# Kernel tuning notes

Measured on AMD Instinct MI355X. Metric: run time of the kernel, lower is better.

## Reference

```python
import jax, jax.numpy as jnp
import numpy as np

N, E, B = 20000, 60000, 512
F_IN, ED, H, C = 7, 3, 4, 256
HC = H * C  # 1024
D_MODEL = 1024
EPS_BN = 1e-5


def setup_inputs() -> dict:
    key = jax.random.key(0)
    ks = jax.random.split(key, 24)
    s = 0.05
    inp = {
        'x': jax.random.normal(ks[0], (N, F_IN), jnp.float32),
        'edge_index': jax.random.randint(ks[1], (2, E), 0, N, jnp.int32),
        'edge_attr': jax.random.normal(ks[2], (E, ED), jnp.float32),
        'batch': jnp.sort(jax.random.randint(ks[3], (N,), 0, B, jnp.int32)),
        'w0': jax.random.normal(ks[4], (F_IN, HC), jnp.float32) * s,
        'w_rest': jax.random.normal(ks[5], (3, HC, HC), jnp.float32) * s,
        'w_edge': jax.random.normal(ks[6], (4, ED, HC), jnp.float32) * s,
        'att_src': jax.random.normal(ks[7], (4, H, C), jnp.float32) * s,
        'att_dst': jax.random.normal(ks[8], (4, H, C), jnp.float32) * s,
        'att_edge': jax.random.normal(ks[9], (4, H, C), jnp.float32) * s,
        'bias012': jax.random.normal(ks[10], (3, HC), jnp.float32) * s,
        'bias3': jax.random.normal(ks[11], (C,), jnp.float32) * s,
        'bn_gamma': jnp.ones((3, HC), jnp.float32),
        'bn_beta': jnp.zeros((3, HC), jnp.float32),
        'bn_mean': jnp.zeros((3, HC), jnp.float32),
        'bn_var': jnp.ones((3, HC), jnp.float32),
        'gate_w': jax.random.normal(ks[12], (C, 1), jnp.float32) * s,
        'gate_b': jnp.zeros((1,), jnp.float32),
        'proj_w': jax.random.normal(ks[13], (C, D_MODEL), jnp.float32) * s,
        'proj_b': jnp.zeros((D_MODEL,), jnp.float32),
    }
    return inp


def _gat_layer(x, ei, ea, W, We, a_s, a_d, a_e, bias, concat):
    # PyG GATConv with edge_dim, add_self_loops=True (fill_value='mean'), eval mode (no dropout)
    n = x.shape[0]
    sl = jnp.arange(n, dtype=ei.dtype)
    ea_mean = ea.mean(axis=0)
    ei = jnp.concatenate([ei, jnp.stack([sl, sl])], axis=1)            # [2, E+N]
    ea = jnp.concatenate([ea, jnp.broadcast_to(ea_mean, (n, ea.shape[1]))], axis=0)
    h = (x @ W).reshape(n, H, C)                                       # [N,H,C]
    alpha_src = jnp.einsum('nhc,hc->nh', h, a_s)
    alpha_dst = jnp.einsum('nhc,hc->nh', h, a_d)
    eh = (ea @ We).reshape(-1, H, C)
    alpha_e = jnp.einsum('ehc,hc->eh', eh, a_e)
    src, dst = ei[0], ei[1]
    alpha = jax.nn.leaky_relu(alpha_src[src] + alpha_dst[dst] + alpha_e, 0.2)  # [E+N,H]
    amax = jax.ops.segment_max(alpha, dst, num_segments=n)
    alpha = jnp.exp(alpha - amax[dst])
    denom = jax.ops.segment_sum(alpha, dst, num_segments=n)
    alpha = alpha / (denom[dst] + 1e-16)
    msg = h[src] * alpha[:, :, None]                                   # [E+N,H,C]
    out = jax.ops.segment_sum(msg, dst, num_segments=n)                # [N,H,C]
    out = out.reshape(n, H * C) if concat else out.mean(axis=1)
    return out + bias


def reference(x, edge_index, edge_attr, batch, w0, w_rest, w_edge, att_src, att_dst,
              att_edge, bias012, bias3, bn_gamma, bn_beta, bn_mean, bn_var,
              gate_w, gate_b, proj_w, proj_b):
    h = x
    for i in range(4):
        W = w0 if i == 0 else w_rest[i - 1]
        concat = i < 3
        b = bias012[i] if concat else bias3
        h = _gat_layer(h, edge_index, edge_attr, W, w_edge[i],
                       att_src[i], att_dst[i], att_edge[i], b, concat)
        if i < 3:
            # BatchNorm1d in eval mode, then ReLU (dropout is identity in eval)
            h = (h - bn_mean[i]) * (bn_gamma[i] / jnp.sqrt(bn_var[i] + EPS_BN)) + bn_beta[i]
            h = jax.nn.relu(h)
    # AttentionalAggregation: segment softmax over gate scores, weighted sum per graph
    gate = h @ gate_w + gate_b                                         # [N,1]
    gmax = jax.ops.segment_max(gate, batch, num_segments=B)
    g = jnp.exp(gate - gmax[batch])
    gsum = jax.ops.segment_sum(g, batch, num_segments=B)
    w = g / (gsum[batch] + 1e-16)
    graph = jax.ops.segment_sum(w * h, batch, num_segments=B)          # [B,256]
    return graph @ proj_w + proj_b                                     # [B,1024]
```

## Files before the change

kernel.cpp:

```cpp
#include <hip/hip_runtime.h>
#include <math.h>

#define NN 20000
#define NP 20480
#define EE 60000
#define BB 512
#define HC 1024
#define HH 4
#define CC 256

typedef _Float16 f16;
typedef f16 half8 __attribute__((ext_vector_type(8)));
typedef f16 f16x4 __attribute__((ext_vector_type(4)));
typedef float floatx4 __attribute__((ext_vector_type(4)));
typedef float floatx16 __attribute__((ext_vector_type(16)));

__device__ __forceinline__ size_t af_off(int n, int c) {
    int mblk = n >> 7, rr = n & 127;
    int iter = c >> 5, kc = c & 31;
    int kh = kc >> 4, kg = (kc >> 3) & 1, e = kc & 7;
    return ((((size_t)(mblk * 32 + iter) * 2 + kh) * 4 + (rr >> 5)) * 64 +
            (kg * 32 + (rr & 31))) * 8 + e;
}

__global__ void ea_sum_kernel(const float* __restrict__ ea, float* sums, int E_) {
    float s0 = 0.f, s1 = 0.f, s2 = 0.f;
    for (int e = blockIdx.x * 256 + threadIdx.x; e < E_; e += gridDim.x * 256) {
        s0 += ea[e * 3 + 0];
        s1 += ea[e * 3 + 1];
        s2 += ea[e * 3 + 2];
    }
    for (int o = 32; o; o >>= 1) {
        s0 += __shfl_down(s0, o);
        s1 += __shfl_down(s1, o);
        s2 += __shfl_down(s2, o);
    }
    if ((threadIdx.x & 63) == 0) {
        atomicAdd(&sums[0], s0);
        atomicAdd(&sums[1], s1);
        atomicAdd(&sums[2], s2);
    }
}

__global__ void hist_kernel(const int* __restrict__ ei, int* counts, int E_) {
    int e = blockIdx.x * 256 + threadIdx.x;
    if (e < E_) atomicAdd(&counts[ei[E_ + e]], 1);
}

__global__ void scan1_kernel(const int* __restrict__ counts, int* __restrict__ partial,
                             int* __restrict__ psums, int n) {
    __shared__ int sdata[256];
    int t = threadIdx.x;
    int i = blockIdx.x * 256 + t;
    int v = (i < n) ? counts[i] : 0;
    sdata[t] = v;
    __syncthreads();
#pragma unroll
    for (int off = 1; off < 256; off <<= 1) {
        int tmp = (t >= off) ? sdata[t - off] : 0;
        __syncthreads();
        sdata[t] += tmp;
        __syncthreads();
    }
    if (i < n) partial[i] = sdata[t];
    if (t == 255) psums[blockIdx.x] = sdata[255];
}

__global__ void scan2_kernel(int* __restrict__ psums, int nb) {
    __shared__ int sdata[128];
    int t = threadIdx.x;
    sdata[t] = (t < nb) ? psums[t] : 0;
    __syncthreads();
#pragma unroll
    for (int off = 1; off < 128; off <<= 1) {
        int tmp = (t >= off) ? sdata[t - off] : 0;
        __syncthreads();
        sdata[t] += tmp;
        __syncthreads();
    }
    if (t < nb) psums[t] = (t == 0) ? 0 : sdata[t - 1];
}

__global__ void scan3_kernel(const int* __restrict__ partial, const int* __restrict__ psums,
                             int* __restrict__ indptr, int n) {
    int i = blockIdx.x * 256 + threadIdx.x;
    if (i == 0) indptr[0] = 0;
    if (i < n) indptr[i + 1] = partial[i] + psums[blockIdx.x];
}

__global__ void scatter_kernel(const int* __restrict__ ei, const int* __restrict__ indptr,
                               int* fill, int* sorted, int* sdst, int E_) {
    int e = blockIdx.x * 256 + threadIdx.x;
    if (e >= E_) return;
    int d = ei[E_ + e];
    int pos = indptr[d] + atomicAdd(&fill[d], 1);
    sorted[pos] = e;
    sdst[pos] = d;
}

__global__ void bptr_kernel(const int* __restrict__ batch, int* bptr, int n, int nb) {
    int i = blockIdx.x * 256 + threadIdx.x;
    if (i >= n) return;
    int b = batch[i];
    if (i == 0) {
        for (int bb = 0; bb <= b; bb++) bptr[bb] = 0;
    } else {
        int pb = batch[i - 1];
        if (pb != b) {
            for (int bb = pb + 1; bb <= b; bb++) bptr[bb] = i;
        }
    }
    if (i == n - 1) {
        for (int bb = b + 1; bb <= nb; bb++) bptr[bb] = n;
    }
}

__global__ void wconv_kernel(const float* __restrict__ w_rest, f16* __restrict__ wt) {
    __shared__ float tile[64][65];
    int l = blockIdx.z;
    int bx = blockIdx.x * 64;
    int by = blockIdx.y * 64;
    int t = threadIdx.x;
    int tr = t >> 6, tc = t & 63;
#pragma unroll
    for (int i = 0; i < 16; i++) {
        int r = by + i * 4 + tr;
        tile[i * 4 + tr][tc] = w_rest[(size_t)l * 1048576 + (size_t)r * 1024 + bx + tc];
    }
    __syncthreads();
#pragma unroll
    for (int i = 0; i < 16; i++) {
        int n = bx + i * 4 + tr;
        wt[(size_t)l * 1048576 + (size_t)n * 1024 + by + tc] = (f16)tile[tc][i * 4 + tr];
    }
}

__global__ void bfrs_kernel(const f16* __restrict__ wt, f16* __restrict__ Bf) {
    int iter = blockIdx.x, nblk = blockIdx.y, l = blockIdx.z;
    const f16* wl = wt + (size_t)l * 1048576;
    f16* bl = Bf + (size_t)l * 1048576;
    int t = threadIdx.x;
    for (int c = t; c < 512; c += 256) {
        int kh = c >> 8, rem = c & 255, cg = rem >> 6, lane = rem & 63;
        int n = nblk * 128 + cg * 32 + (lane & 31);
        int k = iter * 32 + (kh * 2 + (lane >> 5)) * 8;
        half8 v = *(const half8*)&wl[(size_t)n * 1024 + k];
        *(half8*)&bl[(size_t)(nblk * 32 + iter) * 4096 + c * 8] = v;
    }
}

__global__ void mmat_all_kernel(const float* __restrict__ w_edge,
                                const float* __restrict__ att_edge,
                                const float* __restrict__ ea_sums, float* Mmat,
                                float* ae_self, float invE) {
    __shared__ float red[256];
    __shared__ float Ms[12];
    int l = blockIdx.x;
    int t = threadIdx.x;
    for (int dh = 0; dh < 12; dh++) {
        int d = dh >> 2, hh = dh & 3;
        float v = w_edge[l * 3072 + d * HC + hh * CC + t] * att_edge[l * HC + hh * CC + t];
        red[t] = v;
        __syncthreads();
        for (int o = 128; o; o >>= 1) {
            if (t < o) red[t] += red[t + o];
            __syncthreads();
        }
        if (t == 0) {
            Ms[dh] = red[0];
            Mmat[l * 12 + dh] = red[0];
        }
        __syncthreads();
    }
    if (t < 4) {
        float v = 0.f;
        for (int d = 0; d < 3; d++) v += ea_sums[d] * invE * Ms[d * 4 + t];
        ae_self[l * 4 + t] = v;
    }
}

__global__ void pack_kernel(const int* __restrict__ ei, const int* __restrict__ sorted,
                            const float* __restrict__ ea, const float* __restrict__ Mmat,
                            int* __restrict__ ssrc, float* __restrict__ aeh_pk) {
    int idx = blockIdx.x * 256 + threadIdx.x;
    if (idx >= EE) return;
    int eid = sorted[idx];
    ssrc[idx] = ei[eid];
    float a0 = ea[eid * 3 + 0], a1 = ea[eid * 3 + 1], a2 = ea[eid * 3 + 2];
#pragma unroll
    for (int l = 0; l < 4; l++) {
#pragma unroll
        for (int h = 0; h < 4; h++) {
            aeh_pk[(size_t)idx * 16 + l * 4 + h] =
                a0 * Mmat[l * 12 + h] + a1 * Mmat[l * 12 + 4 + h] + a2 * Mmat[l * 12 + 8 + h];
        }
    }
}

__global__ void edgep_kernel(const int* __restrict__ ssrc, const int* __restrict__ sdst,
                             const float* __restrict__ aeh_pk, const float* __restrict__ asrc,
                             const float* __restrict__ adst, float* __restrict__ pe,
                             int layer) {
    int i = blockIdx.x * 256 + threadIdx.x;
    if (i >= EE) return;
    int src = ssrc[i];
    int dst = sdst[i];
    float4 a = *(const float4*)&asrc[(size_t)src * 4];
    float4 d = *(const float4*)&adst[(size_t)dst * 4];
    float4 m = *(const float4*)&aeh_pk[(size_t)i * 16 + layer * 4];
    float r[4] = {a.x + d.x + m.x, a.y + d.y + m.y, a.z + d.z + m.z, a.w + d.w + m.w};
    float4 o;
#pragma unroll
    for (int k = 0; k < 4; k++) {
        float v = (r[k] > 0.f) ? r[k] : 0.2f * r[k];
        (&o.x)[k] = __expf(v);
    }
    *(float4*)&pe[(size_t)i * 4] = o;
}

__global__ void bnss_kernel(const float* __restrict__ bias012, const float* __restrict__ bn_g,
                            const float* __restrict__ bn_b, const float* __restrict__ bn_m,
                            const float* __restrict__ bn_v, float2* __restrict__ bnss) {
    int i = blockIdx.x * 256 + threadIdx.x;
    if (i >= 3 * HC) return;
    float s = bn_g[i] * rsqrtf(bn_v[i] + 1e-5f);
    float2 o;
    o.x = s;
    o.y = (bias012[i] - bn_m[i]) * s + bn_b[i];
    bnss[i] = o;
}

__global__ void wvec_kernel(const float* __restrict__ w_rest, const float* __restrict__ att_src,
                            const float* __restrict__ att_dst, float* __restrict__ wsv,
                            float* __restrict__ wdv) {
    int l = blockIdx.y;
    int k = blockIdx.x;
    int t = threadIdx.x;
    int hp = t >> 6, lane = t & 63;
    int col = hp * 256 + lane * 4;
    const float* wrow = w_rest + (size_t)l * 1048576 + (size_t)k * 1024;
    float4 w4 = *(const float4*)&wrow[col];
    float4 a4 = *(const float4*)&att_src[(l + 1) * HC + col];
    float4 d4 = *(const float4*)&att_dst[(l + 1) * HC + col];
    float sp = w4.x * a4.x + w4.y * a4.y + w4.z * a4.z + w4.w * a4.w;
    float dp = w4.x * d4.x + w4.y * d4.y + w4.z * d4.z + w4.w * d4.w;
    for (int m = 1; m < 64; m <<= 1) {
        sp += __shfl_xor(sp, m);
        dp += __shfl_xor(dp, m);
    }
    if (lane == 0) {
        wsv[((size_t)l * 1024 + k) * 4 + hp] = sp;
        wdv[((size_t)l * 1024 + k) * 4 + hp] = dp;
    }
}

__global__ void w0vec_kernel(const float* __restrict__ w0, const float* __restrict__ att_src,
                             const float* __restrict__ att_dst, float* __restrict__ w0s,
                             float* __restrict__ w0d) {
    int f = blockIdx.x;
    int t = threadIdx.x;
    int hp = t >> 6, lane = t & 63;
    int col = hp * 256 + lane * 4;
    float4 w4 = *(const float4*)&w0[f * HC + col];
    float4 a4 = *(const float4*)&att_src[col];
    float4 d4 = *(const float4*)&att_dst[col];
    float sp = w4.x * a4.x + w4.y * a4.y + w4.z * a4.z + w4.w * a4.w;
    float dp = w4.x * d4.x + w4.y * d4.y + w4.z * d4.z + w4.w * d4.w;
    for (int m = 1; m < 64; m <<= 1) {
        sp += __shfl_xor(sp, m);
        dp += __shfl_xor(dp, m);
    }
    if (lane == 0) {
        w0s[f * 4 + hp] = sp;
        w0d[f * 4 + hp] = dp;
    }
}

__global__ void alpha0_kernel(const float* __restrict__ x, const float* __restrict__ w0s,
                              const float* __restrict__ w0d, float* __restrict__ asrc,
                              float* __restrict__ adst) {
    int n = blockIdx.x * 256 + threadIdx.x;
    if (n >= NN) return;
    float xr[7];
#pragma unroll
    for (int f = 0; f < 7; f++) xr[f] = x[n * 7 + f];
#pragma unroll
    for (int hp = 0; hp < 4; hp++) {
        float s = 0.f, d = 0.f;
#pragma unroll
        for (int f = 0; f < 7; f++) {
            s += xr[f] * w0s[f * 4 + hp];
            d += xr[f] * w0d[f * 4 + hp];
        }
        asrc[n * 4 + hp] = s;
        adst[n * 4 + hp] = d;
    }
}

__global__ void agg0x_kernel(const float* __restrict__ x, const float* __restrict__ asrc,
                             const float* __restrict__ adst, const float* __restrict__ ae_self,
                             const int* __restrict__ ssrc, const float* __restrict__ pe,
                             const int* __restrict__ indptr, float* __restrict__ xagg) {
    int n = blockIdx.x * 256 + threadIdx.x;
    if (n >= NN) return;
    float4 as4 = *(const float4*)&asrc[(size_t)n * 4];
    float4 ad4 = *(const float4*)&adst[(size_t)n * 4];
    float adl[4] = {ad4.x, ad4.y, ad4.z, ad4.w};
    float asl[4] = {as4.x, as4.y, as4.z, as4.w};
    float xr[7];
#pragma unroll
    for (int f = 0; f < 7; f++) xr[f] = x[n * 7 + f];
    float denom[4];
    float xa[4][7];
#pragma unroll
    for (int h = 0; h < 4; h++) {
        float r = asl[h] + adl[h] + ae_self[h];
        r = (r > 0.f) ? r : 0.2f * r;
        float p = __expf(r);
        denom[h] = p;
#pragma unroll
        for (int f = 0; f < 7; f++) xa[h][f] = p * xr[f];
    }
    int s = indptr[n], e = indptr[n + 1];
    for (int idx = s; idx < e; idx++) {
        int src = ssrc[idx];
        float4 pv = *(const float4*)&pe[(size_t)idx * 4];
        float pl[4] = {pv.x, pv.y, pv.z, pv.w};
        float xs[7];
#pragma unroll
        for (int f = 0; f < 7; f++) xs[f] = x[src * 7 + f];
#pragma unroll
        for (int h = 0; h < 4; h++) {
            denom[h] += pl[h];
#pragma unroll
            for (int f = 0; f < 7; f++) xa[h][f] += pl[h] * xs[f];
        }
    }
#pragma unroll
    for (int h = 0; h < 4; h++) {
        float inv = 1.0f / (denom[h] + 1e-16f);
#pragma unroll
        for (int f = 0; f < 7; f++) xagg[(size_t)n * 28 + h * 7 + f] = xa[h][f] * inv;
    }
}

__global__ void gemm7f_kernel(const float* __restrict__ xagg, const float* __restrict__ w0,
                              const float2* __restrict__ bnss, const float* __restrict__ wsv,
                              const float* __restrict__ wdv, f16* __restrict__ outAf,
                              float* __restrict__ asrc_n, float* __restrict__ adst_n) {
    __shared__ float xs[28];
    __shared__ float red[32];
    int n = blockIdx.x, t = threadIdx.x;
    if (t < 28) xs[t] = xagg[(size_t)n * 28 + t];
    __syncthreads();
    int head = t >> 6;
    int j0 = t * 4;
    float sp[4] = {0.f, 0.f, 0.f, 0.f}, dp[4] = {0.f, 0.f, 0.f, 0.f};
    f16x4 o;
#pragma unroll
    for (int k = 0; k < 4; k++) {
        int j = j0 + k;
        float dot = 0.f;
#pragma unroll
        for (int f = 0; f < 7; f++) dot += xs[head * 7 + f] * w0[f * HC + j];
        float2 ss = bnss[j];
        float val = fmaxf(fmaf(dot, ss.x, ss.y), 0.f);
        o[k] = (f16)val;
        float4 w4s = *(const float4*)&wsv[(size_t)j * 4];
        float4 w4d = *(const float4*)&wdv[(size_t)j * 4];
        sp[0] += val * w4s.x; sp[1] += val * w4s.y;
        sp[2] += val * w4s.z; sp[3] += val * w4s.w;
        dp[0] += val * w4d.x; dp[1] += val * w4d.y;
        dp[2] += val * w4d.z; dp[3] += val * w4d.w;
    }
    *(f16x4*)&outAf[af_off(n, j0)] = o;
    int wave = t >> 6, lane = t & 63;
#pragma unroll
    for (int m = 1; m < 64; m <<= 1) {
#pragma unroll
        for (int j = 0; j < 4; j++) {
            sp[j] += __shfl_xor(sp[j], m);
            dp[j] += __shfl_xor(dp[j], m);
        }
    }
    if (lane == 0) {
#pragma unroll
        for (int j = 0; j < 4; j++) {
            red[wave * 8 + j] = sp[j];
            red[wave * 8 + 4 + j] = dp[j];
        }
    }
    __syncthreads();
    if (t < 8) {
        float v = red[t] + red[8 + t] + red[16 + t] + red[24 + t];
        if (t < 4) asrc_n[n * 4 + t] = v;
        else adst_n[n * 4 + (t - 4)] = v;
    }
}

__global__ __launch_bounds__(256) void mfma_gemm_kernel(const f16* __restrict__ Af,
                                                        const f16* __restrict__ Bf,
                                                        f16* __restrict__ C16) {
    int t = threadIdx.x;
    int wave = t >> 6, lane = t & 63;
    int gid = blockIdx.x;
    int g = gid >> 6, rblk = gid & 63;
    int nblk = rblk >> 3;
    int mblk = g * 8 + (rblk & 7);
    int rg0 = (wave >> 1) * 2;
    int cg0 = (wave & 1) * 2;

    floatx16 acc[2][2];
#pragma unroll
    for (int i = 0; i < 2; i++)
#pragma unroll
        for (int j = 0; j < 2; j++) acc[i][j] = (floatx16)(0.f);

    const f16* pa = Af + (size_t)mblk * 131072 + (size_t)lane * 8;
    const f16* pb = Bf + (size_t)nblk * 131072 + (size_t)lane * 8;

#pragma unroll 2
    for (int iter = 0; iter < 32; iter++) {
        size_t base = (size_t)iter * 4096;
        half8 afr[2][2], bfr[2][2];
#pragma unroll
        for (int kh = 0; kh < 2; kh++) {
#pragma unroll
            for (int i = 0; i < 2; i++) {
                afr[kh][i] = *(const half8*)&pa[base + kh * 2048 + (rg0 + i) * 512];
                bfr[kh][i] = *(const half8*)&pb[base + kh * 2048 + (cg0 + i) * 512];
            }
        }
#pragma unroll
        for (int kh = 0; kh < 2; kh++)
#pragma unroll
            for (int i = 0; i < 2; i++)
#pragma unroll
                for (int j = 0; j < 2; j++)
                    acc[i][j] = __builtin_amdgcn_mfma_f32_32x32x16_f16(bfr[kh][j], afr[kh][i],
                                                                       acc[i][j], 0, 0, 0);
    }

    int fr32 = lane & 31, kg = lane >> 5;
#pragma unroll
    for (int i = 0; i < 2; i++) {
        int row = mblk * 128 + rg0 * 32 + i * 32 + fr32;
#pragma unroll
        for (int j = 0; j < 2; j++) {
#pragma unroll
            for (int gq = 0; gq < 4; gq++) {
                f16x4 o;
#pragma unroll
                for (int r = 0; r < 4; r++) o[r] = (f16)acc[i][j][gq * 4 + r];
                *(f16x4*)&C16[(size_t)row * HC + nblk * 128 + cg0 * 32 + j * 32 + gq * 8 +
                              kg * 4] = o;
            }
        }
    }
}

__global__ void agg_kernel(const f16* __restrict__ h16, const float* __restrict__ asrc,
                           const float* __restrict__ adst, const float* __restrict__ ae_self,
                           const int* __restrict__ ssrc, const float* __restrict__ pe,
                           const int* __restrict__ indptr, const float2* __restrict__ bnss,
                           const float* __restrict__ wsv, const float* __restrict__ wdv,
                           const float* __restrict__ bias3, const float* __restrict__ gw,
                           const float* __restrict__ gb, f16* __restrict__ out16,
                           float* __restrict__ asrc_n, float* __restrict__ adst_n,
                           float* __restrict__ out3, float* __restrict__ gate,
                           int layer, int concat) {
    __shared__ float buf[1024];
    __shared__ float red[32];
    int n = blockIdx.x, t = threadIdx.x;
    int h = t >> 6, lane = t & 63;
    int c4 = t * 4;

    float r = asrc[n * 4 + h] + adst[n * 4 + h] + ae_self[layer * 4 + h];
    r = (r > 0.f) ? r : 0.2f * r;
    float p = __expf(r);
    float denom = p;
    float ax, ay, az, aw;
    {
        f16x4 v = *(const f16x4*)&h16[(size_t)n * HC + c4];
        ax = p * (float)v[0]; ay = p * (float)v[1];
        az = p * (float)v[2]; aw = p * (float)v[3];
    }
    int s = indptr[n], epos = indptr[n + 1];
    for (int base = s; base < epos; base += 4) {
        int rem = epos - base;
        int src[4];
        float pv[4];
#pragma unroll
        for (int j = 0; j < 4; j++) {
            if (j < rem) {
                src[j] = ssrc[base + j];
                pv[j] = pe[(size_t)(base + j) * 4 + h];
            } else {
                src[j] = n;
                pv[j] = 0.f;
            }
        }
        f16x4 u[4];
#pragma unroll
        for (int j = 0; j < 4; j++) u[j] = *(const f16x4*)&h16[(size_t)src[j] * HC + c4];
#pragma unroll
        for (int j = 0; j < 4; j++) {
            denom += pv[j];
            ax += pv[j] * (float)u[j][0];
            ay += pv[j] * (float)u[j][1];
            az += pv[j] * (float)u[j][2];
            aw += pv[j] * (float)u[j][3];
        }
    }
    float inv = 1.0f / (denom + 1e-16f);
    ax *= inv; ay *= inv; az *= inv; aw *= inv;

    if (concat) {
        float vals[4] = {ax, ay, az, aw};
        f16x4 o;
        float sp[4] = {0.f, 0.f, 0.f, 0.f}, dp[4] = {0.f, 0.f, 0.f, 0.f};
#pragma unroll
        for (int k = 0; k < 4; k++) {
            int j = c4 + k;
            float2 ss = bnss[j];
            float val = fmaxf(fmaf(vals[k], ss.x, ss.y), 0.f);
            o[k] = (f16)val;
            float4 w4s = *(const float4*)&wsv[(size_t)j * 4];
            float4 w4d = *(const float4*)&wdv[(size_t)j * 4];
            sp[0] += val * w4s.x; sp[1] += val * w4s.y;
            sp[2] += val * w4s.z; sp[3] += val * w4s.w;
            dp[0] += val * w4d.x; dp[1] += val * w4d.y;
            dp[2] += val * w4d.z; dp[3] += val * w4d.w;
        }
        *(f16x4*)&out16[af_off(n, c4)] = o;
#pragma unroll
        for (int m = 1; m < 64; m <<= 1) {
#pragma unroll
            for (int j = 0; j < 4; j++) {
                sp[j] += __shfl_xor(sp[j], m);
                dp[j] += __shfl_xor(dp[j], m);
            }
        }
        if (lane == 0) {
#pragma unroll
            for (int j = 0; j < 4; j++) {
                red[h * 8 + j] = sp[j];
                red[h * 8 + 4 + j] = dp[j];
            }
        }
        __syncthreads();
        if (t < 8) {
            float v = red[t] + red[8 + t] + red[16 + t] + red[24 + t];
            if (t < 4) asrc_n[n * 4 + t] = v;
            else adst_n[n * 4 + (t - 4)] = v;
        }
    } else {
        buf[c4 + 0] = ax;
        buf[c4 + 1] = ay;
        buf[c4 + 2] = az;
        buf[c4 + 3] = aw;
        __syncthreads();
        if (t < 64) {
            float gpart = 0.f;
#pragma unroll
            for (int k = 0; k < 4; k++) {
                int c = t * 4 + k;
                float v2 = 0.25f * (buf[c] + buf[256 + c] + buf[512 + c] + buf[768 + c]) +
                           bias3[c];
                out3[(size_t)n * CC + c] = v2;
                gpart += v2 * gw[c];
            }
            for (int o = 32; o; o >>= 1) gpart += __shfl_down(gpart, o);
            if (t == 0) gate[n] = gpart + gb[0];
        }
    }
}

__global__ void graphagg_kernel(const float* __restrict__ gate, const float* __restrict__ h3,
                                const int* __restrict__ bptr, float* __restrict__ graph) {
    __shared__ float red[256];
    __shared__ float wn[256];
    int b = blockIdx.x, t = threadIdx.x;
    int s = bptr[b], epos = bptr[b + 1];
    float m = -3.4e38f;
    for (int n = s + t; n < epos; n += 256) m = fmaxf(m, gate[n]);
    red[t] = m;
    __syncthreads();
    for (int o = 128; o; o >>= 1) {
        if (t < o) red[t] = fmaxf(red[t], red[t + o]);
        __syncthreads();
    }
    float mval = red[0];
    __syncthreads();
    float sum = 0.f;
    for (int n = s + t; n < epos; n += 256) sum += __expf(gate[n] - mval);
    red[t] = sum;
    __syncthreads();
    for (int o = 128; o; o >>= 1) {
        if (t < o) red[t] += red[t + o];
        __syncthreads();
    }
    float ssum = red[0];
    __syncthreads();
    float acc = 0.f;
    for (int base = s; base < epos; base += 256) {
        int n = base + t;
        wn[t] = (n < epos) ? __expf(gate[n] - mval) : 0.f;
        __syncthreads();
        int cnt = min(256, epos - base);
        for (int j = 0; j < cnt; j++) acc += wn[j] * h3[(size_t)(base + j) * CC + t];
        __syncthreads();
    }
    graph[b * CC + t] = acc / (ssum + 1e-16f);
}

__global__ void proj_kernel(const float* __restrict__ graph, const float* __restrict__ pw,
                            const float* __restrict__ pb, float* __restrict__ out) {
    __shared__ float g[256];
    int b = blockIdx.x, t = threadIdx.x;
    g[t] = graph[b * CC + t];
    __syncthreads();
    for (int j = t; j < 1024; j += 256) {
        float acc = pb[j];
        for (int c = 0; c < 256; c++) acc += g[c] * pw[c * 1024 + j];
        out[(size_t)b * 1024 + j] = acc;
    }
}

extern "C" void kernel_launch(void* const* d_in, const int* in_sizes, int n_in,
                              void* d_out, int out_size, void* d_ws, size_t ws_size,
                              hipStream_t stream) {
    const float* x = (const float*)d_in[0];
    const int* ei = (const int*)d_in[1];
    const float* ea = (const float*)d_in[2];
    const int* batch = (const int*)d_in[3];
    const float* w0 = (const float*)d_in[4];
    const float* w_rest = (const float*)d_in[5];
    const float* w_edge = (const float*)d_in[6];
    const float* att_src = (const float*)d_in[7];
    const float* att_dst = (const float*)d_in[8];
    const float* att_edge = (const float*)d_in[9];
    const float* bias012 = (const float*)d_in[10];
    const float* bias3 = (const float*)d_in[11];
    const float* bn_g = (const float*)d_in[12];
    const float* bn_b = (const float*)d_in[13];
    const float* bn_m = (const float*)d_in[14];
    const float* bn_v = (const float*)d_in[15];
    const float* gate_w = (const float*)d_in[16];
    const float* gate_b = (const float*)d_in[17];
    const float* proj_w = (const float*)d_in[18];
    const float* proj_b = (const float*)d_in[19];
    float* out = (float*)d_out;

    float* ws = (float*)d_ws;
    size_t off = 0;
    f16* h_lin = (f16*)(ws + off); off += (size_t)NP * HC / 2;
    f16* h_af = (f16*)(ws + off); off += (size_t)NP * HC / 2;
    float* h3 = ws + off; off += (size_t)NN * CC;
    f16* wt = (f16*)(ws + off); off += (size_t)3 * HC * HC / 2;
    f16* Bf = (f16*)(ws + off); off += (size_t)3 * HC * HC / 2;
    float* asrcA = ws + off; off += (size_t)NN * 4;
    float* adstA = ws + off; off += (size_t)NN * 4;
    float* asrcB = ws + off; off += (size_t)NN * 4;
    float* adstB = ws + off; off += (size_t)NN * 4;
    float* wsv = ws + off; off += (size_t)3 * HC * 4;
    float* wdv = ws + off; off += (size_t)3 * HC * 4;
    float* w0s = ws + off; off += 28;
    float* w0d = ws + off; off += 28;
    float2* bnss = (float2*)(ws + off); off += (size_t)3 * HC * 2;
    float* aeh_pk = ws + off; off += (size_t)EE * 16;
    float* pbuf = ws + off; off += (size_t)EE * 4;
    float* xagg = ws + off; off += (size_t)NN * 28;
    float* gate = ws + off; off += (size_t)NN;
    float* graph = ws + off; off += (size_t)BB * CC;
    float* ea_sums = ws + off; off += 4;
    float* Mmat = ws + off; off += 48;
    float* ae_self = ws + off; off += 16;
    int* counts = (int*)(ws + off); off += NN;
    int* partial = (int*)(ws + off); off += NN;
    int* psums = (int*)(ws + off); off += 128;
    int* indptr = (int*)(ws + off); off += NN + 1;
    int* fill = (int*)(ws + off); off += NN;
    int* sorted = (int*)(ws + off); off += EE;
    int* ssrc = (int*)(ws + off); off += EE;
    int* sdst = (int*)(ws + off); off += EE;
    int* bptr = (int*)(ws + off); off += BB + 1;

    hipMemsetAsync(ea_sums, 0, 4 * sizeof(float), stream);
    hipMemsetAsync(counts, 0, NN * sizeof(int), stream);
    hipMemsetAsync(fill, 0, NN * sizeof(int), stream);

    ea_sum_kernel<<<64, 256, 0, stream>>>(ea, ea_sums, EE);
    hist_kernel<<<(EE + 255) / 256, 256, 0, stream>>>(ei, counts, EE);
    int nblk = (NN + 255) / 256;
    scan1_kernel<<<nblk, 256, 0, stream>>>(counts, partial, psums, NN);
    scan2_kernel<<<1, 128, 0, stream>>>(psums, nblk);
    scan3_kernel<<<nblk, 256, 0, stream>>>(partial, psums, indptr, NN);
    scatter_kernel<<<(EE + 255) / 256, 256, 0, stream>>>(ei, indptr, fill, sorted, sdst, EE);
    bptr_kernel<<<(NN + 255) / 256, 256, 0, stream>>>(batch, bptr, NN, BB);
    wconv_kernel<<<dim3(16, 16, 3), 256, 0, stream>>>(w_rest, wt);
    bfrs_kernel<<<dim3(32, 8, 3), 256, 0, stream>>>(wt, Bf);
    mmat_all_kernel<<<4, 256, 0, stream>>>(w_edge, att_edge, ea_sums, Mmat, ae_self,
                                           1.0f / EE);
    pack_kernel<<<(EE + 255) / 256, 256, 0, stream>>>(ei, sorted, ea, Mmat, ssrc, aeh_pk);
    bnss_kernel<<<(3 * HC + 255) / 256, 256, 0, stream>>>(bias012, bn_g, bn_b, bn_m, bn_v,
                                                          bnss);
    wvec_kernel<<<dim3(1024, 3), 256, 0, stream>>>(w_rest, att_src, att_dst, wsv, wdv);
    w0vec_kernel<<<7, 256, 0, stream>>>(w0, att_src, att_dst, w0s, w0d);
    alpha0_kernel<<<(NN + 255) / 256, 256, 0, stream>>>(x, w0s, w0d, asrcA, adstA);

    edgep_kernel<<<(EE + 255) / 256, 256, 0, stream>>>(ssrc, sdst, aeh_pk, asrcA, adstA,
                                                       pbuf, 0);
    agg0x_kernel<<<(NN + 255) / 256, 256, 0, stream>>>(x, asrcA, adstA, ae_self, ssrc,
                                                       pbuf, indptr, xagg);
    gemm7f_kernel<<<NN, 256, 0, stream>>>(xagg, w0, bnss, wsv, wdv, h_af, asrcB, adstB);

    float* asrc_cur = asrcB;
    float* adst_cur = adstB;
    float* asrc_nxt = asrcA;
    float* adst_nxt = adstA;
    for (int i = 1; i < 4; i++) {
        mfma_gemm_kernel<<<(NP / 128) * (HC / 128), 256, 0, stream>>>(
            h_af, Bf + (size_t)(i - 1) * HC * HC, h_lin);
        edgep_kernel<<<(EE + 255) / 256, 256, 0, stream>>>(ssrc, sdst, aeh_pk, asrc_cur,
                                                           adst_cur, pbuf, i);
        agg_kernel<<<NN, 256, 0, stream>>>(
            h_lin, asrc_cur, adst_cur, ae_self, ssrc, pbuf, indptr, bnss + (size_t)i * HC,
            wsv + (size_t)i * HC * 4, wdv + (size_t)i * HC * 4, bias3, gate_w, gate_b,
            h_af, asrc_nxt, adst_nxt, h3, gate, i, (i < 3) ? 1 : 0);
        float* tmp = asrc_cur; asrc_cur = asrc_nxt; asrc_nxt = tmp;
        tmp = adst_cur; adst_cur = adst_nxt; adst_nxt = tmp;
    }

    graphagg_kernel<<<BB, 256, 0, stream>>>(gate, h3, bptr, graph);
    proj_kernel<<<BB, 256, 0, stream>>>(graph, proj_w, proj_b, out);
}
```

Measured before the change: 680.6 us.

## Fuse weight prep kernels, pad x, widen gather unroll, tile projection

Merges the weight transpose and fragment reshuffle into one kernel that writes the MFMA layout directly, which drops the intermediate f16 buffer. It also folds the bnss, wvec and w0vec prep kernels into a single launch. Node features are padded to 8 floats so the layer-0 gathers can use float4 loads. The per-edge gather loop in the aggregation kernel now unrolls over 8 edges instead of 4, and the final projection handles 8 graphs per block so each weight load is reused. Together these aim to cut launch count, memory traffic and latency in the preprocessing and aggregation paths, at the cost of more registers per thread.

Measured after the change: 682.3 us. Within noise of the previous version (+0.2%).

```diff
diff --git a/kernel.cpp b/kernel.cpp
--- a/kernel.cpp
+++ b/kernel.cpp
@@ -115,7 +115,7 @@
     }
 }
 
-__global__ void wconv_kernel(const float* __restrict__ w_rest, f16* __restrict__ wt) {
+__global__ void wbf_kernel(const float* __restrict__ w_rest, f16* __restrict__ Bf) {
     __shared__ float tile[64][65];
     int l = blockIdx.z;
     int bx = blockIdx.x * 64;
@@ -128,24 +128,16 @@
         tile[i * 4 + tr][tc] = w_rest[(size_t)l * 1048576 + (size_t)r * 1024 + bx + tc];
     }
     __syncthreads();
-#pragma unroll
-    for (int i = 0; i < 16; i++) {
-        int n = bx + i * 4 + tr;
-        wt[(size_t)l * 1048576 + (size_t)n * 1024 + by + tc] = (f16)tile[tc][i * 4 + tr];
-    }
-}
-
-__global__ void bfrs_kernel(const f16* __restrict__ wt, f16* __restrict__ Bf) {
-    int iter = blockIdx.x, nblk = blockIdx.y, l = blockIdx.z;
-    const f16* wl = wt + (size_t)l * 1048576;
     f16* bl = Bf + (size_t)l * 1048576;
-    int t = threadIdx.x;
-    for (int c = t; c < 512; c += 256) {
-        int kh = c >> 8, rem = c & 255, cg = rem >> 6, lane = rem & 63;
-        int n = nblk * 128 + cg * 32 + (lane & 31);
-        int k = iter * 32 + (kh * 2 + (lane >> 5)) * 8;
-        half8 v = *(const half8*)&wl[(size_t)n * 1024 + k];
-        *(half8*)&bl[(size_t)(nblk * 32 + iter) * 4096 + c * 8] = v;
+#pragma unroll
+    for (int ii = 0; ii < 2; ii++) {
+        int idx = ii * 256 + t;
+        int nl = idx >> 3, kg8 = idx & 7;
+        int n = bx + nl, k = by + kg8 * 8;
+        half8 v;
+#pragma unroll
+        for (int e = 0; e < 8; e++) v[e] = (f16)tile[kg8 * 8 + e][nl];
+        *(half8*)&bl[af_off(n, k)] = v;
     }
 }
 
@@ -218,72 +210,78 @@
     *(float4*)&pe[(size_t)i * 4] = o;
 }
 
-__global__ void bnss_kernel(const float* __restrict__ bias012, const float* __restrict__ bn_g,
-                            const float* __restrict__ bn_b, const float* __restrict__ bn_m,
-                            const float* __restrict__ bn_v, float2* __restrict__ bnss) {
-    int i = blockIdx.x * 256 + threadIdx.x;
-    if (i >= 3 * HC) return;
-    float s = bn_g[i] * rsqrtf(bn_v[i] + 1e-5f);
-    float2 o;
-    o.x = s;
-    o.y = (bias012[i] - bn_m[i]) * s + bn_b[i];
-    bnss[i] = o;
-}
-
-__global__ void wvec_kernel(const float* __restrict__ w_rest, const float* __restrict__ att_src,
-                            const float* __restrict__ att_dst, float* __restrict__ wsv,
-                            float* __restrict__ wdv) {
-    int l = blockIdx.y;
-    int k = blockIdx.x;
+__global__ void prep1_kernel(const float* __restrict__ w_rest,
+                             const float* __restrict__ att_src,
+                             const float* __restrict__ att_dst,
+                             const float* __restrict__ w0,
+                             const float* __restrict__ bias012, const float* __restrict__ bn_g,
+                             const float* __restrict__ bn_b, const float* __restrict__ bn_m,
+                             const float* __restrict__ bn_v,
+                             float* __restrict__ wsv, float* __restrict__ wdv,
+                             float* __restrict__ w0s, float* __restrict__ w0d,
+                             float2* __restrict__ bnss) {
+    int b = blockIdx.x;
     int t = threadIdx.x;
-    int hp = t >> 6, lane = t & 63;
-    int col = hp * 256 + lane * 4;
-    const float* wrow = w_rest + (size_t)l * 1048576 + (size_t)k * 1024;
-    float4 w4 = *(const float4*)&wrow[col];
-    float4 a4 = *(const float4*)&att_src[(l + 1) * HC + col];
-    float4 d4 = *(const float4*)&att_dst[(l + 1) * HC + col];
-    float sp = w4.x * a4.x + w4.y * a4.y + w4.z * a4.z + w4.w * a4.w;
-    float dp = w4.x * d4.x + w4.y * d4.y + w4.z * d4.z + w4.w * d4.w;
-    for (int m = 1; m < 64; m <<= 1) {
-        sp += __shfl_xor(sp, m);
-        dp += __shfl_xor(dp, m);
-    }
-    if (lane == 0) {
-        wsv[((size_t)l * 1024 + k) * 4 + hp] = sp;
-        wdv[((size_t)l * 1024 + k) * 4 + hp] = dp;
-    }
-}
-
-__global__ void w0vec_kernel(const float* __restrict__ w0, const float* __restrict__ att_src,
-                             const float* __restrict__ att_dst, float* __restrict__ w0s,
-                             float* __restrict__ w0d) {
-    int f = blockIdx.x;
-    int t = threadIdx.x;
-    int hp = t >> 6, lane = t & 63;
-    int col = hp * 256 + lane * 4;
-    float4 w4 = *(const float4*)&w0[f * HC + col];
-    float4 a4 = *(const float4*)&att_src[col];
-    float4 d4 = *(const float4*)&att_dst[col];
-    float sp = w4.x * a4.x + w4.y * a4.y + w4.z * a4.z + w4.w * a4.w;
-    float dp = w4.x * d4.x + w4.y * d4.y + w4.z * d4.z + w4.w * d4.w;
-    for (int m = 1; m < 64; m <<= 1) {
-        sp += __shfl_xor(sp, m);
-        dp += __shfl_xor(dp, m);
-    }
-    if (lane == 0) {
-        w0s[f * 4 + hp] = sp;
-        w0d[f * 4 + hp] = dp;
+    if (b < 3072) {
+        int l = b >> 10, k = b & 1023;
+        int hp = t >> 6, lane = t & 63;
+        int col = hp * 256 + lane * 4;
+        const float* wrow = w_rest + (size_t)l * 1048576 + (size_t)k * 1024;
+        float4 w4 = *(const float4*)&wrow[col];
+        float4 a4 = *(const float4*)&att_src[(l + 1) * HC + col];
+        float4 d4 = *(const float4*)&att_dst[(l + 1) * HC + col];
+        float sp = w4.x * a4.x + w4.y * a4.y + w4.z * a4.z + w4.w * a4.w;
+        float dp = w4.x * d4.x + w4.y * d4.y + w4.z * d4.z + w4.w * d4.w;
+        for (int m = 1; m < 64; m <<= 1) {
+            sp += __shfl_xor(sp, m);
+            dp += __shfl_xor(dp, m);
+        }
+        if (lane == 0) {
+            wsv[((size_t)l * 1024 + k) * 4 + hp] = sp;
+            wdv[((size_t)l * 1024 + k) * 4 + hp] = dp;
+        }
+    } else if (b < 3079) {
+        int f = b - 3072;
+        int hp = t >> 6, lane = t & 63;
+        int col = hp * 256 + lane * 4;
+        float4 w4 = *(const float4*)&w0[f * HC + col];
+        float4 a4 = *(const float4*)&att_src[col];
+        float4 d4 = *(const float4*)&att_dst[col];
+        float sp = w4.x * a4.x + w4.y * a4.y + w4.z * a4.z + w4.w * a4.w;
+        float dp = w4.x * d4.x + w4.y * d4.y + w4.z * d4.z + w4.w * d4.w;
+        for (int m = 1; m < 64; m <<= 1) {
+            sp += __shfl_xor(sp, m);
+            dp += __shfl_xor(dp, m);
+        }
+        if (lane == 0) {
+            w0s[f * 4 + hp] = sp;
+            w0d[f * 4 + hp] = dp;
+        }
+    } else {
+        int i = (b - 3079) * 256 + t;
+        if (i < 3 * HC) {
+            float s = bn_g[i] * rsqrtf(bn_v[i] + 1e-5f);
+            float2 o;
+            o.x = s;
+            o.y = (bias012[i] - bn_m[i]) * s + bn_b[i];
+            bnss[i] = o;
+        }
     }
 }
 
 __global__ void alpha0_kernel(const float* __restrict__ x, const float* __restrict__ w0s,
                               const float* __restrict__ w0d, float* __restrict__ asrc,
-                              float* __restrict__ adst) {
+                              float* __restrict__ adst, float* __restrict__ xpad) {
     int n = blockIdx.x * 256 + threadIdx.x;
     if (n >= NN) return;
     float xr[7];
 #pragma unroll
     for (int f = 0; f < 7; f++) xr[f] = x[n * 7 + f];
+    float4 p0, p1;
+    p0.x = xr[0]; p0.y = xr[1]; p0.z = xr[2]; p0.w = xr[3];
+    p1.x = xr[4]; p1.y = xr[5]; p1.z = xr[6]; p1.w = 0.f;
+    *(float4*)&xpad[(size_t)n * 8] = p0;
+    *(float4*)&xpad[(size_t)n * 8 + 4] = p1;
 #pragma unroll
     for (int hp = 0; hp < 4; hp++) {
         float s = 0.f, d = 0.f;
@@ -297,7 +295,7 @@
     }
 }
 
-__global__ void agg0x_kernel(const float* __restrict__ x, const float* __restrict__ asrc,
+__global__ void agg0x_kernel(const float* __restrict__ xpad, const float* __restrict__ asrc,
                              const float* __restrict__ adst, const float* __restrict__ ae_self,
                              const int* __restrict__ ssrc, const float* __restrict__ pe,
                              const int* __restrict__ indptr, float* __restrict__ xagg) {
@@ -307,9 +305,9 @@
     float4 ad4 = *(const float4*)&adst[(size_t)n * 4];
     float adl[4] = {ad4.x, ad4.y, ad4.z, ad4.w};
     float asl[4] = {as4.x, as4.y, as4.z, as4.w};
-    float xr[7];
-#pragma unroll
-    for (int f = 0; f < 7; f++) xr[f] = x[n * 7 + f];
+    float4 x0 = *(const float4*)&xpad[(size_t)n * 8];
+    float4 x1 = *(const float4*)&xpad[(size_t)n * 8 + 4];
+    float xr[7] = {x0.x, x0.y, x0.z, x0.w, x1.x, x1.y, x1.z};
     float denom[4];
     float xa[4][7];
 #pragma unroll
@@ -326,9 +324,9 @@
         int src = ssrc[idx];
         float4 pv = *(const float4*)&pe[(size_t)idx * 4];
         float pl[4] = {pv.x, pv.y, pv.z, pv.w};
-        float xs[7];
-#pragma unroll
-        for (int f = 0; f < 7; f++) xs[f] = x[src * 7 + f];
+        float4 s0 = *(const float4*)&xpad[(size_t)src * 8];
+        float4 s1 = *(const float4*)&xpad[(size_t)src * 8 + 4];
+        float xs[7] = {s0.x, s0.y, s0.z, s0.w, s1.x, s1.y, s1.z};
 #pragma unroll
         for (int h = 0; h < 4; h++) {
             denom[h] += pl[h];
@@ -486,12 +484,12 @@
         az = p * (float)v[2]; aw = p * (float)v[3];
     }
     int s = indptr[n], epos = indptr[n + 1];
-    for (int base = s; base < epos; base += 4) {
+    for (int base = s; base < epos; base += 8) {
         int rem = epos - base;
-        int src[4];
-        float pv[4];
-#pragma unroll
-        for (int j = 0; j < 4; j++) {
+        int src[8];
+        float pv[8];
+#pragma unroll
+        for (int j = 0; j < 8; j++) {
             if (j < rem) {
                 src[j] = ssrc[base + j];
                 pv[j] = pe[(size_t)(base + j) * 4 + h];
@@ -500,11 +498,11 @@
                 pv[j] = 0.f;
             }
         }
-        f16x4 u[4];
-#pragma unroll
-        for (int j = 0; j < 4; j++) u[j] = *(const f16x4*)&h16[(size_t)src[j] * HC + c4];
-#pragma unroll
-        for (int j = 0; j < 4; j++) {
+        f16x4 u[8];
+#pragma unroll
+        for (int j = 0; j < 8; j++) u[j] = *(const f16x4*)&h16[(size_t)src[j] * HC + c4];
+#pragma unroll
+        for (int j = 0; j < 8; j++) {
             denom += pv[j];
             ax += pv[j] * (float)u[j][0];
             ay += pv[j] * (float)u[j][1];
@@ -616,15 +614,32 @@
 
 __global__ void proj_kernel(const float* __restrict__ graph, const float* __restrict__ pw,
                             const float* __restrict__ pb, float* __restrict__ out) {
-    __shared__ float g[256];
+    __shared__ float g[8][256];
     int b = blockIdx.x, t = threadIdx.x;
-    g[t] = graph[b * CC + t];
-    __syncthreads();
-    for (int j = t; j < 1024; j += 256) {
-        float acc = pb[j];
-        for (int c = 0; c < 256; c++) acc += g[c] * pw[c * 1024 + j];
-        out[(size_t)b * 1024 + j] = acc;
-    }
+#pragma unroll
+    for (int r = 0; r < 8; r++) g[r][t] = graph[(size_t)(b * 8 + r) * 256 + t];
+    __syncthreads();
+    float acc[8][4];
+#pragma unroll
+    for (int r = 0; r < 8; r++)
+#pragma unroll
+        for (int q = 0; q < 4; q++) acc[r][q] = pb[t + q * 256];
+    for (int c = 0; c < 256; c++) {
+        float w[4];
+#pragma unroll
+        for (int q = 0; q < 4; q++) w[q] = pw[(size_t)c * 1024 + t + q * 256];
+#pragma unroll
+        for (int r = 0; r < 8; r++) {
+            float gv = g[r][c];
+#pragma unroll
+            for (int q = 0; q < 4; q++) acc[r][q] += gv * w[q];
+        }
+    }
+#pragma unroll
+    for (int r = 0; r < 8; r++)
+#pragma unroll
+        for (int q = 0; q < 4; q++)
+            out[(size_t)(b * 8 + r) * 1024 + t + q * 256] = acc[r][q];
 }
 
 extern "C" void kernel_launch(void* const* d_in, const int* in_sizes, int n_in,
@@ -657,8 +672,8 @@
     f16* h_lin = (f16*)(ws + off); off += (size_t)NP * HC / 2;
     f16* h_af = (f16*)(ws + off); off += (size_t)NP * HC / 2;
     float* h3 = ws + off; off += (size_t)NN * CC;
-    f16* wt = (f16*)(ws + off); off += (size_t)3 * HC * HC / 2;
     f16* Bf = (f16*)(ws + off); off += (size_t)3 * HC * HC / 2;
+    float* xpad = ws + off; off += (size_t)NN * 8;
     float* asrcA = ws + off; off += (size_t)NN * 4;
     float* adstA = ws + off; off += (size_t)NN * 4;
     float* asrcB = ws + off; off += (size_t)NN * 4;
@@ -698,20 +713,17 @@
     scan3_kernel<<<nblk, 256, 0, stream>>>(partial, psums, indptr, NN);
     scatter_kernel<<<(EE + 255) / 256, 256, 0, stream>>>(ei, indptr, fill, sorted, sdst, EE);
     bptr_kernel<<<(NN + 255) / 256, 256, 0, stream>>>(batch, bptr, NN, BB);
-    wconv_kernel<<<dim3(16, 16, 3), 256, 0, stream>>>(w_rest, wt);
-    bfrs_kernel<<<dim3(32, 8, 3), 256, 0, stream>>>(wt, Bf);
+    wbf_kernel<<<dim3(16, 16, 3), 256, 0, stream>>>(w_rest, Bf);
     mmat_all_kernel<<<4, 256, 0, stream>>>(w_edge, att_edge, ea_sums, Mmat, ae_self,
                                            1.0f / EE);
     pack_kernel<<<(EE + 255) / 256, 256, 0, stream>>>(ei, sorted, ea, Mmat, ssrc, aeh_pk);
-    bnss_kernel<<<(3 * HC + 255) / 256, 256, 0, stream>>>(bias012, bn_g, bn_b, bn_m, bn_v,
-                                                          bnss);
-    wvec_kernel<<<dim3(1024, 3), 256, 0, stream>>>(w_rest, att_src, att_dst, wsv, wdv);
-    w0vec_kernel<<<7, 256, 0, stream>>>(w0, att_src, att_dst, w0s, w0d);
-    alpha0_kernel<<<(NN + 255) / 256, 256, 0, stream>>>(x, w0s, w0d, asrcA, adstA);
+    prep1_kernel<<<3091, 256, 0, stream>>>(w_rest, att_src, att_dst, w0, bias012, bn_g,
+                                           bn_b, bn_m, bn_v, wsv, wdv, w0s, w0d, bnss);
+    alpha0_kernel<<<(NN + 255) / 256, 256, 0, stream>>>(x, w0s, w0d, asrcA, adstA, xpad);
 
     edgep_kernel<<<(EE + 255) / 256, 256, 0, stream>>>(ssrc, sdst, aeh_pk, asrcA, adstA,
                                                        pbuf, 0);
-    agg0x_kernel<<<(NN + 255) / 256, 256, 0, stream>>>(x, asrcA, adstA, ae_self, ssrc,
+    agg0x_kernel<<<(NN + 255) / 256, 256, 0, stream>>>(xpad, asrcA, adstA, ae_self, ssrc,
                                                        pbuf, indptr, xagg);
     gemm7f_kernel<<<NN, 256, 0, stream>>>(xagg, w0, bnss, wsv, wdv, h_af, asrcB, adstB);
 
@@ -733,5 +745,5 @@
     }
 
     graphagg_kernel<<<BB, 256, 0, stream>>>(gate, h3, bptr, graph);
-    proj_kernel<<<BB, 256, 0, stream>>>(graph, proj_w, proj_b, out);
-}
+    proj_kernel<<<BB / 8, 256, 0, stream>>>(graph, proj_w, proj_b, out);
+}
```
